# Optimization experiments

Measured on AMD Instinct MI355X. Metric: run time of the kernel, lower is better.

Reference implementation:

```python
import jax, jax.numpy as jnp
import numpy as np

K = 3
K2 = K * K


def conv2d(x, w, b, stride=1, pad=0):
    y = jax.lax.conv_general_dilated(
        x, w, (stride, stride), [(pad, pad), (pad, pad)],
        dimension_numbers=('NCHW', 'OIHW', 'NCHW'))
    return y + b[None, :, None, None]


def bilinear_gather(x, ys, xs):
    # x: [B,C,H,W]; ys,xs: [B,K2,H,W] float coords; zero outside bounds (torchvision deform_conv2d semantics)
    B, C, H, W = x.shape
    y0 = jnp.floor(ys)
    x0 = jnp.floor(xs)
    fy = (ys - y0)[:, None]  # [B,1,K2,H,W]
    fx = (xs - x0)[:, None]
    xf = x.reshape(B, C, H * W)

    def gather(yc, xc):
        valid = (yc >= 0) & (yc <= H - 1) & (xc >= 0) & (xc <= W - 1)
        yi = jnp.clip(yc, 0, H - 1).astype(jnp.int32)
        xi = jnp.clip(xc, 0, W - 1).astype(jnp.int32)
        idx = (yi * W + xi).reshape(B, 1, -1)
        g = jnp.take_along_axis(xf, idx, axis=2).reshape(B, C, K2, H, W)
        return g * valid[:, None].astype(x.dtype)

    g00 = gather(y0, x0)
    g01 = gather(y0, x0 + 1)
    g10 = gather(y0 + 1, x0)
    g11 = gather(y0 + 1, x0 + 1)
    return (g00 * (1 - fy) * (1 - fx) + g01 * (1 - fy) * fx
            + g10 * fy * (1 - fx) + g11 * fy * fx)


def deform_conv(x, w_off, b_off, w, b):
    # DCNv1: offsets predicted by a regular 3x3 conv, then 3x3 conv over bilinearly sampled taps
    B, C, H, W = x.shape
    pad = 1
    off = conv2d(x, w_off, b_off, pad=pad).reshape(B, K2, 2, H, W)  # (dy,dx) per tap
    ky, kx = jnp.meshgrid(jnp.arange(K), jnp.arange(K), indexing='ij')
    base_y = jnp.arange(H)[None, None, :, None] + (ky.reshape(K2) - pad)[None, :, None, None]
    base_x = jnp.arange(W)[None, None, None, :] + (kx.reshape(K2) - pad)[None, :, None, None]
    ys = base_y + off[:, :, 0]
    xs = base_x + off[:, :, 1]
    samples = bilinear_gather(x, ys, xs)  # [B,C,K2,H,W]
    out = jnp.einsum('bckhw,ock->bohw', samples, w.reshape(w.shape[0], C, K2))
    return out + b[None, :, None, None]


def band_high_mask(h, w):
    y, x = jnp.meshgrid(jnp.arange(h), jnp.arange(w), indexing='ij')
    d = jnp.sqrt(((y - h // 2) ** 2 + (x - w // 2) ** 2).astype(jnp.float32))
    return (d > h // 16).astype(jnp.float32)


def reference(x, w1, b1, ws, bs, wb, bb, woff, boff, wreg, breg, w2, b2):
    B, Cin, Hx, Wx = x.shape
    c0 = conv2d(x, w1, b1)                                  # 1x1 reduce
    c1 = conv2d(c0, ws, bs, stride=2, pad=0)                # 3x3 s2 p0 -> 111x111
    c1 = jax.lax.reduce_window(c1, -jnp.inf, jax.lax.max,
                               (1, 1, 7, 7), (1, 1, 3, 3), 'VALID')  # -> 35x35
    f = jnp.fft.fftshift(jnp.fft.fft2(c1, axes=(-2, -1)), axes=(-2, -1))
    mag = jnp.abs(f)
    phase = jnp.angle(f)
    h, w = mag.shape[-2], mag.shape[-1]
    hb = mag * band_high_mask(h, w)
    for l in range(3):  # fixed structural loop over the 3 DCN+ReLU blocks
        hb = jax.nn.relu(deform_conv(hb, woff[l], boff[l], wreg[l], breg[l]))
    rec = jax.lax.complex(hb * jnp.cos(phase), hb * jnp.sin(phase))
    rec = jnp.real(jnp.fft.ifft2(jnp.fft.ifftshift(rec, axes=(-2, -1)), axes=(-2, -1)))
    up = jax.image.resize(rec, (B, rec.shape[1], Hx, Wx), method='bilinear')  # align_corners=False
    c2 = jax.nn.sigmoid(conv2d(conv2d(c0, wb, bb) + up, w2, b2))
    return x * c2


def setup_inputs():
    key = jax.random.key(0)
    ks = jax.random.split(key, 8)
    B, Cin, H, W = 4, 256, 224, 224
    Cr = Cin // 8
    f32 = jnp.float32
    x = jax.random.normal(ks[0], (B, Cin, H, W), f32)
    w1 = jax.random.normal(ks[1], (Cr, Cin, 1, 1), f32) * 0.05
    b1 = jnp.zeros((Cr,), f32)
    ws = jax.random.normal(ks[2], (Cr, Cr, 3, 3), f32) * 0.05
    bs = jnp.zeros((Cr,), f32)
    wb = jax.random.normal(ks[3], (Cr, Cr, 1, 1), f32) * 0.05
    bb = jnp.zeros((Cr,), f32)
    woff = jax.random.normal(ks[4], (3, 2 * K2, Cr, 3, 3), f32) * 0.002  # small -> moderate offsets
    boff = jnp.zeros((3, 2 * K2), f32)
    wreg = jax.random.normal(ks[5], (3, Cr, Cr, 3, 3), f32) * 0.05
    breg = jnp.zeros((3, Cr), f32)
    w2 = jax.random.normal(ks[6], (Cin, Cr, 1, 1), f32) * 0.05
    b2 = jnp.zeros((Cin,), f32)
    return dict(x=x, w1=w1, b1=b1, ws=ws, bs=bs, wb=wb, bb=bb,
                woff=woff, boff=boff, wreg=wreg, breg=breg, w2=w2, b2=b2)
```

## Files before the change

kernel.cpp:

```cpp
#include <hip/hip_runtime.h>
#include <math.h>

#define PI_F 3.14159265358979323846f

#define BATCH 4
#define CIN 256
#define CR 32
#define H0 224
#define HW0 (224*224)
#define H1 111
#define HW1 (111*111)
#define HS 35
#define HWS (35*35)

typedef short bf16x8 __attribute__((ext_vector_type(8)));
typedef float f32x4 __attribute__((ext_vector_type(4)));
typedef unsigned int u32x4 __attribute__((ext_vector_type(4)));

__device__ inline unsigned pack2(float a, float b) {
  unsigned ua = __builtin_bit_cast(unsigned, a);
  unsigned ub = __builtin_bit_cast(unsigned, b);
  return ((ua + 0x8000u) >> 16) | (((ub + 0x8000u) >> 16) << 16);
}

__device__ inline bf16x8 pack8(const float f[8]) {
  u32x4 u;
  u[0] = pack2(f[0], f[1]);
  u[1] = pack2(f[2], f[3]);
  u[2] = pack2(f[4], f[5]);
  u[3] = pack2(f[6], f[7]);
  return __builtin_bit_cast(bf16x8, u);
}

__global__ __launch_bounds__(256) void k_prep(
    const float* __restrict__ w1, const float* __restrict__ b1,
    const float* __restrict__ wb, const float* __restrict__ bb,
    float* __restrict__ Wcat, float* __restrict__ bias_v) {
  __shared__ float wbl[32 * 32];
  int t = threadIdx.x;
  for (int i = t; i < 1024; i += 256) wbl[i] = wb[i];
  __syncthreads();
  float col[32];
#pragma unroll
  for (int m = 0; m < 32; ++m) col[m] = w1[m * CIN + t];
#pragma unroll
  for (int o = 0; o < 32; ++o) {
    float s = 0.f;
#pragma unroll
    for (int m = 0; m < 32; ++m) s = fmaf(wbl[o * 32 + m], col[m], s);
    Wcat[o * CIN + t] = s;
  }
  if (t < 32) {
    float s = bb[t];
#pragma unroll
    for (int m = 0; m < 32; ++m) s = fmaf(wbl[t * 32 + m], b1[m], s);
    bias_v[t] = s;
  }
}

__global__ __launch_bounds__(256) void k_conv1x1(
    const float* __restrict__ x, const float* __restrict__ w1,
    const float* __restrict__ b1, const float* __restrict__ Wcat,
    const float* __restrict__ bias_v,
    float* __restrict__ c0, float* __restrict__ v0) {
  int tid = threadIdx.x, lane = tid & 63, wid = tid >> 6;
  int l15 = lane & 15, lg = lane >> 4;
  int pxg = blockIdx.x * 256 + wid * 64;
  int b = pxg / HW0, p0 = pxg % HW0;
  f32x4 acc[4][4];
#pragma unroll
  for (int ct = 0; ct < 4; ++ct)
#pragma unroll
    for (int pt = 0; pt < 4; ++pt)
#pragma unroll
      for (int r = 0; r < 4; ++r) acc[ct][pt][r] = 0.f;
  const float* xb = x + (size_t)b * CIN * HW0 + p0 + l15;
  for (int ks = 0; ks < 8; ++ks) {
    bf16x8 Bf[4];
#pragma unroll
    for (int pt = 0; pt < 4; ++pt) {
      const float* xp = xb + (size_t)(ks * 32 + lg * 8) * HW0 + pt * 16;
      float f[8];
#pragma unroll
      for (int j = 0; j < 8; ++j) f[j] = xp[(size_t)j * HW0];
      Bf[pt] = pack8(f);
    }
    bf16x8 A[4];
#pragma unroll
    for (int ct = 0; ct < 4; ++ct) {
      const float* base = (ct < 2)
          ? w1 + (ct * 16 + l15) * CIN
          : Wcat + ((ct - 2) * 16 + l15) * CIN;
      const float* wr = base + ks * 32 + lg * 8;
      float f[8];
      float4 a0 = *reinterpret_cast<const float4*>(wr);
      float4 a1 = *reinterpret_cast<const float4*>(wr + 4);
      f[0]=a0.x; f[1]=a0.y; f[2]=a0.z; f[3]=a0.w;
      f[4]=a1.x; f[5]=a1.y; f[6]=a1.z; f[7]=a1.w;
      A[ct] = pack8(f);
    }
#pragma unroll
    for (int ct = 0; ct < 4; ++ct)
#pragma unroll
      for (int pt = 0; pt < 4; ++pt)
        acc[ct][pt] = __builtin_amdgcn_mfma_f32_16x16x32_bf16(
            A[ct], Bf[pt], acc[ct][pt], 0, 0, 0);
  }
#pragma unroll
  for (int ct = 0; ct < 4; ++ct) {
    int co = (ct & 1) * 16 + lg * 4;
    float bias[4];
#pragma unroll
    for (int r = 0; r < 4; ++r)
      bias[r] = (ct < 2) ? b1[co + r] : bias_v[co + r];
    float* dst = (ct < 2) ? c0 : v0;
    float* ob = dst + ((size_t)b * CR + co) * HW0 + p0 + l15;
#pragma unroll
    for (int pt = 0; pt < 4; ++pt)
#pragma unroll
      for (int r = 0; r < 4; ++r)
        ob[(size_t)r * HW0 + pt * 16] = acc[ct][pt][r] + bias[r];
  }
}

#define PPR 56
#define PAIRS_B (H1 * PPR)
#define PAIRS_T (BATCH * PAIRS_B)
#define C3_THREADS (PAIRS_T * 4)
__global__ __launch_bounds__(256) void k_conv3x3s2(
    const float* __restrict__ c0, const float* __restrict__ wsw,
    const float* __restrict__ bs, float* __restrict__ c1) {
  __shared__ float wl[288 * 32];
  int tid = threadIdx.x;
  for (int i = tid; i < 9216; i += 256) {
    int o = i & 31, r = i >> 5;
    wl[i] = wsw[o * 288 + r];
  }
  __syncthreads();
  int T = blockIdx.x * 256 + tid;
  if (T >= C3_THREADS) return;
  int og = T / PAIRS_T;
  int pair = T % PAIRS_T;
  int b = pair / PAIRS_B;
  int pr = pair % PAIRS_B;
  int y = pr / PPR, xp = pr % PPR;
  bool tail = (xp == PPR - 1);
  const float* ibase = c0 + (size_t)b * CR * HW0 + (2 * y) * H0 + 4 * xp;
  float acc0[8], acc1[8];
#pragma unroll
  for (int j = 0; j < 8; ++j) { acc0[j] = 0.f; acc1[j] = 0.f; }
  for (int ci = 0; ci < CR; ++ci) {
    float p[3][5];
#pragma unroll
    for (int ky = 0; ky < 3; ++ky) {
      const float* rp = ibase + (size_t)ci * HW0 + ky * H0;
      float4 v = *reinterpret_cast<const float4*>(rp);
      p[ky][0] = v.x; p[ky][1] = v.y; p[ky][2] = v.z; p[ky][3] = v.w;
      p[ky][4] = tail ? 0.f : rp[4];
    }
    const float* wbase = &wl[ci * 9 * 32 + og * 8];
#pragma unroll
    for (int k = 0; k < 9; ++k) {
      int ky = k / 3, kx = k % 3;
      float4 wa = *reinterpret_cast<const float4*>(wbase + k * 32);
      float4 wc = *reinterpret_cast<const float4*>(wbase + k * 32 + 4);
      float wv[8] = {wa.x, wa.y, wa.z, wa.w, wc.x, wc.y, wc.z, wc.w};
      float pa = p[ky][kx], pb = p[ky][kx + 2];
#pragma unroll
      for (int j = 0; j < 8; ++j) {
        acc0[j] = fmaf(pa, wv[j], acc0[j]);
        acc1[j] = fmaf(pb, wv[j], acc1[j]);
      }
    }
  }
  float* ob = c1 + (size_t)b * CR * HW1 + y * H1 + 2 * xp;
  int o0 = og * 8;
#pragma unroll
  for (int j = 0; j < 8; ++j) {
    float bias = bs[o0 + j];
    ob[(size_t)(o0 + j) * HW1] = acc0[j] + bias;
    if (!tail) ob[(size_t)(o0 + j) * HW1 + 1] = acc1[j] + bias;
  }
}

__global__ __launch_bounds__(512) void k_fft(
    const float* __restrict__ c1, float* __restrict__ hb,
    float* __restrict__ cph, float* __restrict__ sph) {
  __shared__ float p[HWS];
  __shared__ float Tr[HWS], Ti[HWS];
  __shared__ float twc[HS], tws[HS];
  int img = blockIdx.x;
  const float* cb = c1 + (size_t)img * HW1;
  for (int i = threadIdx.x; i < HWS; i += 512) {
    int y = i / HS, x = i % HS;
    const float* ip = cb + (3 * y) * H1 + 3 * x;
    float m = -INFINITY;
#pragma unroll
    for (int ky = 0; ky < 7; ++ky)
#pragma unroll
      for (int kx = 0; kx < 7; ++kx)
        m = fmaxf(m, ip[ky * H1 + kx]);
    p[i] = m;
  }
  if (threadIdx.x < HS) {
    float ang = -2.f * PI_F * (float)threadIdx.x / (float)HS;
    twc[threadIdx.x] = cosf(ang);
    tws[threadIdx.x] = sinf(ang);
  }
  __syncthreads();
  for (int i = threadIdx.x; i < HWS; i += 512) {
    int u = i / HS, xx = i % HS;
    float sr = 0.f, si = 0.f;
    int t = 0;
    for (int y = 0; y < HS; ++y) {
      float v = p[y * HS + xx];
      sr = fmaf(v, twc[t], sr);
      si = fmaf(v, tws[t], si);
      t += u; if (t >= HS) t -= HS;
    }
    Tr[i] = sr; Ti[i] = si;
  }
  __syncthreads();
  float* hp = hb + (size_t)img * HWS;
  float* cp = cph + (size_t)img * HWS;
  float* sp = sph + (size_t)img * HWS;
  for (int i = threadIdx.x; i < HWS; i += 512) {
    int oy = i / HS, ox = i % HS;
    int u = oy + 18; if (u >= HS) u -= HS;
    int v = ox + 18; if (v >= HS) v -= HS;
    float fr = 0.f, fi = 0.f;
    int t = 0;
    for (int xx = 0; xx < HS; ++xx) {
      float tr = Tr[u * HS + xx], ti = Ti[u * HS + xx];
      float c = twc[t], s = tws[t];
      fr += tr * c - ti * s;
      fi += tr * s + ti * c;
      t += v; if (t >= HS) t -= HS;
    }
    float mag = sqrtf(fr * fr + fi * fi);
    float ic = 1.f, is = 0.f;
    if (mag > 0.f) { ic = fr / mag; is = fi / mag; }
    int dy = oy - 17, dx = ox - 17;
    float m = (dy * dy + dx * dx > 4) ? 1.f : 0.f;
    hp[i] = mag * m;
    cp[i] = ic; sp[i] = is;
  }
}

__global__ __launch_bounds__(256) void k_dcn(
    const float* __restrict__ hin, float* __restrict__ hout,
    const float* __restrict__ woff, const float* __restrict__ boff,
    const float* __restrict__ wreg, const float* __restrict__ breg) {
  __shared__ float wo[18 * CR * 9];
  __shared__ float wr[CR * CR * 9];
  __shared__ float bo[18], br[CR];
  for (int i = threadIdx.x; i < 18 * CR * 9; i += 256) wo[i] = woff[i];
  for (int i = threadIdx.x; i < CR * CR * 9; i += 256) wr[i] = wreg[i];
  if (threadIdx.x < 18) bo[threadIdx.x] = boff[threadIdx.x];
  if (threadIdx.x < CR) br[threadIdx.x] = breg[threadIdx.x];
  __syncthreads();
  int pg = threadIdx.x >> 5;
  int sub = threadIdx.x & 31;
  int pid = blockIdx.x * 8 + pg;
  bool active = pid < BATCH * HWS;
  int b = pid / HWS, r = pid % HWS;
  int y = r / HS, x = r % HS;
  const float* ib = hin + (size_t)b * CR * HWS;
  float off[18];
#pragma unroll
  for (int j = 0; j < 18; ++j) off[j] = 0.f;
  if (active) {
    const float* ip = ib + (size_t)sub * HWS;
#pragma unroll
    for (int ky = 0; ky < 3; ++ky) {
      int yy = y + ky - 1;
      if (yy < 0 || yy > HS - 1) continue;
#pragma unroll
      for (int kx = 0; kx < 3; ++kx) {
        int xx = x + kx - 1;
        if (xx < 0 || xx > HS - 1) continue;
        float v = ip[yy * HS + xx];
#pragma unroll
        for (int j = 0; j < 18; ++j)
          off[j] = fmaf(v, wo[(j * CR + sub) * 9 + ky * 3 + kx], off[j]);
      }
    }
  }
#pragma unroll
  for (int d = 1; d < 32; d <<= 1)
#pragma unroll
    for (int j = 0; j < 18; ++j)
      off[j] += __shfl_xor(off[j], d);
#pragma unroll
  for (int j = 0; j < 18; ++j) off[j] += bo[j];
  float acc[CR];
#pragma unroll
  for (int o = 0; o < CR; ++o) acc[o] = 0.f;
  if (active) {
    const float* ip = ib + (size_t)sub * HWS;
#pragma unroll
    for (int k = 0; k < 9; ++k) {
      int ky = k / 3, kx = k % 3;
      float ysf = (float)(y + ky - 1) + off[2 * k];
      float xsf = (float)(x + kx - 1) + off[2 * k + 1];
      float y0 = floorf(ysf), x0 = floorf(xsf);
      float fy = ysf - y0, fx = xsf - x0;
      float y1 = y0 + 1.f, x1 = x0 + 1.f;
      bool vy0 = (y0 >= 0.f) && (y0 <= 34.f);
      bool vy1 = (y1 >= 0.f) && (y1 <= 34.f);
      bool vx0 = (x0 >= 0.f) && (x0 <= 34.f);
      bool vx1 = (x1 >= 0.f) && (x1 <= 34.f);
      int iy0 = (int)fminf(fmaxf(y0, 0.f), 34.f);
      int iy1 = (int)fminf(fmaxf(y1, 0.f), 34.f);
      int ix0 = (int)fminf(fmaxf(x0, 0.f), 34.f);
      int ix1 = (int)fminf(fmaxf(x1, 0.f), 34.f);
      float w00 = (vy0 && vx0) ? (1.f - fy) * (1.f - fx) : 0.f;
      float w01 = (vy0 && vx1) ? (1.f - fy) * fx : 0.f;
      float w10 = (vy1 && vx0) ? fy * (1.f - fx) : 0.f;
      float w11 = (vy1 && vx1) ? fy * fx : 0.f;
      float s = w00 * ip[iy0 * HS + ix0] + w01 * ip[iy0 * HS + ix1]
              + w10 * ip[iy1 * HS + ix0] + w11 * ip[iy1 * HS + ix1];
#pragma unroll
      for (int o = 0; o < CR; ++o)
        acc[o] = fmaf(s, wr[(o * CR + sub) * 9 + k], acc[o]);
    }
  }
#pragma unroll
  for (int d = 1; d < 32; d <<= 1)
#pragma unroll
    for (int o = 0; o < CR; ++o)
      acc[o] += __shfl_xor(acc[o], d);
  if (active) {
    float* ob = hout + (size_t)b * CR * HWS + r;
    float v = acc[sub] + br[sub];
    ob[(size_t)sub * HWS] = fmaxf(v, 0.f);
  }
}

__global__ __launch_bounds__(512) void k_ifft(
    const float* __restrict__ hb, const float* __restrict__ cph,
    const float* __restrict__ sph, float* __restrict__ rec) {
  __shared__ float Gr[HWS], Gi[HWS];
  __shared__ float Tr[HWS], Ti[HWS];
  __shared__ float twc[HS], tws[HS];
  int img = blockIdx.x;
  const float* hp = hb + (size_t)img * HWS;
  const float* cp = cph + (size_t)img * HWS;
  const float* sp = sph + (size_t)img * HWS;
  if (threadIdx.x < HS) {
    float ang = 2.f * PI_F * (float)threadIdx.x / (float)HS;
    twc[threadIdx.x] = cosf(ang);
    tws[threadIdx.x] = sinf(ang);
  }
  for (int i = threadIdx.x; i < HWS; i += 512) {
    int m = i / HS, n = i % HS;
    int sm = m + 17; if (sm >= HS) sm -= HS;
    int sn = n + 17; if (sn >= HS) sn -= HS;
    int si = sm * HS + sn;
    float h = hp[si];
    Gr[i] = h * cp[si];
    Gi[i] = h * sp[si];
  }
  __syncthreads();
  for (int i = threadIdx.x; i < HWS; i += 512) {
    int yy = i / HS, v = i % HS;
    float sr = 0.f, sii = 0.f;
    int t = 0;
    for (int u = 0; u < HS; ++u) {
      float gr = Gr[u * HS + v], gi = Gi[u * HS + v];
      float c = twc[t], s = tws[t];
      sr += gr * c - gi * s;
      sii += gr * s + gi * c;
      t += yy; if (t >= HS) t -= HS;
    }
    Tr[i] = sr; Ti[i] = sii;
  }
  __syncthreads();
  float* rp = rec + (size_t)img * HWS;
  const float inv = 1.f / (float)(HWS);
  for (int i = threadIdx.x; i < HWS; i += 512) {
    int yy = i / HS, xx = i % HS;
    float sr = 0.f;
    int t = 0;
    for (int v = 0; v < HS; ++v) {
      sr += Tr[yy * HS + v] * twc[t] - Ti[yy * HS + v] * tws[t];
      t += xx; if (t >= HS) t -= HS;
    }
    rp[i] = sr * inv;
  }
}

__global__ __launch_bounds__(256) void k_final(
    const float* __restrict__ x, const float* __restrict__ v0buf,
    const float* __restrict__ rec,
    const float* __restrict__ w2, const float* __restrict__ b2,
    float* __restrict__ out) {
  int tid = threadIdx.x, lane = tid & 63, wid = tid >> 6;
  int l15 = lane & 15, lg = lane >> 4;
  int pxg = blockIdx.x * 256 + wid * 64;
  int b = pxg / HW0, p0 = pxg % HW0;
  int ctb = blockIdx.y * 64;
  const float* rb = rec + (size_t)b * CR * HWS;
  const float* vb = v0buf + (size_t)b * CR * HW0 + p0 + l15;
  const float scale = (float)HS / (float)H0;
  bf16x8 Bf[4];
#pragma unroll
  for (int pt = 0; pt < 4; ++pt) {
    int p = p0 + pt * 16 + l15;
    int h = p / H0, wc = p % H0;
    float sy = ((float)h + 0.5f) * scale - 0.5f;
    float sx = ((float)wc + 0.5f) * scale - 0.5f;
    float y0f = floorf(sy), x0f = floorf(sx);
    float fy = sy - y0f, fx = sx - x0f;
    int y0 = max(0, min(HS - 1, (int)y0f));
    int y1 = max(0, min(HS - 1, (int)y0f + 1));
    int x0 = max(0, min(HS - 1, (int)x0f));
    int x1 = max(0, min(HS - 1, (int)x0f + 1));
    float w00 = (1.f - fy) * (1.f - fx), w01 = (1.f - fy) * fx;
    float w10 = fy * (1.f - fx), w11 = fy * fx;
    int i00 = y0 * HS + x0, i01 = y0 * HS + x1;
    int i10 = y1 * HS + x0, i11 = y1 * HS + x1;
    float f[8];
#pragma unroll
    for (int j = 0; j < 8; ++j) {
      const float* rp = rb + (size_t)(lg * 8 + j) * HWS;
      float u = w00 * rp[i00] + w01 * rp[i01] + w10 * rp[i10] + w11 * rp[i11];
      f[j] = vb[(size_t)(lg * 8 + j) * HW0 + pt * 16] + u;
    }
    Bf[pt] = pack8(f);
  }
  bf16x8 A[4];
#pragma unroll
  for (int ct = 0; ct < 4; ++ct) {
    const float* wr = w2 + (ctb + ct * 16 + l15) * CR + lg * 8;
    float f[8];
    float4 a0 = *reinterpret_cast<const float4*>(wr);
    float4 a1 = *reinterpret_cast<const float4*>(wr + 4);
    f[0]=a0.x; f[1]=a0.y; f[2]=a0.z; f[3]=a0.w;
    f[4]=a1.x; f[5]=a1.y; f[6]=a1.z; f[7]=a1.w;
    A[ct] = pack8(f);
  }
  f32x4 acc[4][4];
#pragma unroll
  for (int ct = 0; ct < 4; ++ct)
#pragma unroll
    for (int pt = 0; pt < 4; ++pt)
#pragma unroll
      for (int r = 0; r < 4; ++r) acc[ct][pt][r] = 0.f;
#pragma unroll
  for (int ct = 0; ct < 4; ++ct)
#pragma unroll
    for (int pt = 0; pt < 4; ++pt)
      acc[ct][pt] = __builtin_amdgcn_mfma_f32_16x16x32_bf16(
          A[ct], Bf[pt], acc[ct][pt], 0, 0, 0);
#pragma unroll
  for (int ct = 0; ct < 4; ++ct) {
    int co = ctb + ct * 16 + lg * 4;
    float bias[4];
#pragma unroll
    for (int r = 0; r < 4; ++r) bias[r] = b2[co + r];
    const float* xb = x + ((size_t)b * CIN + co) * HW0 + p0 + l15;
    float* ob = out + ((size_t)b * CIN + co) * HW0 + p0 + l15;
#pragma unroll
    for (int pt = 0; pt < 4; ++pt)
#pragma unroll
      for (int r = 0; r < 4; ++r) {
        float s = acc[ct][pt][r] + bias[r];
        float g = __builtin_amdgcn_rcpf(1.f + __expf(-s));
        ob[(size_t)r * HW0 + pt * 16] = xb[(size_t)r * HW0 + pt * 16] * g;
      }
  }
}

extern "C" void kernel_launch(void* const* d_in, const int* in_sizes, int n_in,
                              void* d_out, int out_size, void* d_ws, size_t ws_size,
                              hipStream_t stream) {
  const float* x    = (const float*)d_in[0];
  const float* w1   = (const float*)d_in[1];
  const float* b1   = (const float*)d_in[2];
  const float* wsw  = (const float*)d_in[3];
  const float* bs   = (const float*)d_in[4];
  const float* wb   = (const float*)d_in[5];
  const float* bb   = (const float*)d_in[6];
  const float* woff = (const float*)d_in[7];
  const float* boff = (const float*)d_in[8];
  const float* wreg = (const float*)d_in[9];
  const float* breg = (const float*)d_in[10];
  const float* w2   = (const float*)d_in[11];
  const float* b2   = (const float*)d_in[12];
  float* out = (float*)d_out;

  float* ws_f = (float*)d_ws;
  float* c0   = ws_f;
  float* v0   = c0 + (size_t)BATCH * CR * HW0;
  float* c1   = v0 + (size_t)BATCH * CR * HW0;
  float* hbA  = c1 + (size_t)BATCH * CR * HW1;
  float* hbB  = hbA + (size_t)BATCH * CR * HWS;
  float* cph  = hbB + (size_t)BATCH * CR * HWS;
  float* sph  = cph + (size_t)BATCH * CR * HWS;
  float* rec  = sph + (size_t)BATCH * CR * HWS;
  float* Wcat = rec + (size_t)BATCH * CR * HWS;
  float* bias_v = Wcat + 32 * CIN;

  k_prep<<<1, 256, 0, stream>>>(w1, b1, wb, bb, Wcat, bias_v);
  k_conv1x1<<<BATCH * HW0 / 256, 256, 0, stream>>>(x, w1, b1, Wcat, bias_v, c0, v0);
  k_conv3x3s2<<<(C3_THREADS + 255) / 256, 256, 0, stream>>>(c0, wsw, bs, c1);
  k_fft<<<BATCH * CR, 512, 0, stream>>>(c1, hbA, cph, sph);
  k_dcn<<<(BATCH * HWS + 7) / 8, 256, 0, stream>>>(hbA, hbB, woff, boff, wreg, breg);
  k_dcn<<<(BATCH * HWS + 7) / 8, 256, 0, stream>>>(hbB, hbA, woff + 5184, boff + 18, wreg + 9216, breg + 32);
  k_dcn<<<(BATCH * HWS + 7) / 8, 256, 0, stream>>>(hbA, hbB, woff + 2 * 5184, boff + 36, wreg + 2 * 9216, breg + 64);
  k_ifft<<<BATCH * CR, 512, 0, stream>>>(hbB, cph, sph, rec);
  dim3 gf(BATCH * HW0 / 256, 4);
  k_final<<<gf, 256, 0, stream>>>(x, v0, rec, w2, b2, out);
}
```

Before: 337.8 us.

## Split FFT/IFFT per image across two blocks, move upsample-add into separate kernel

The FFT and IFFT kernels now launch two blocks per image, each computing only the rows its half of the output needs, so the grid has twice as many blocks. The bilinear upsample of the reconstruction is taken out of the final kernel into a new k_up kernel that adds it into v0 in place. The final MFMA kernel then reads v0 only and covers 32 output channels per block instead of 64, over twice as many blocks. The cost is one extra launch and an extra read-modify-write pass over v0. In exchange the final kernel no longer repeats the upsample for every channel-group block.

```diff
diff --git a/kernel.cpp b/kernel.cpp
--- a/kernel.cpp
+++ b/kernel.cpp
@@ -189,7 +189,11 @@
   __shared__ float p[HWS];
   __shared__ float Tr[HWS], Ti[HWS];
   __shared__ float twc[HS], tws[HS];
-  int img = blockIdx.x;
+  int img = blockIdx.x >> 1;
+  int half = blockIdx.x & 1;
+  int ub = half ? 0 : 18;
+  int un = half ? 18 : 17;
+  int oyb = half ? 17 : 0;
   const float* cb = c1 + (size_t)img * HW1;
   for (int i = threadIdx.x; i < HWS; i += 512) {
     int y = i / HS, x = i % HS;
@@ -208,8 +212,8 @@
     tws[threadIdx.x] = sinf(ang);
   }
   __syncthreads();
-  for (int i = threadIdx.x; i < HWS; i += 512) {
-    int u = i / HS, xx = i % HS;
+  for (int i = threadIdx.x; i < un * HS; i += 512) {
+    int u = ub + i / HS, xx = i % HS;
     float sr = 0.f, si = 0.f;
     int t = 0;
     for (int y = 0; y < HS; ++y) {
@@ -218,14 +222,14 @@
       si = fmaf(v, tws[t], si);
       t += u; if (t >= HS) t -= HS;
     }
-    Tr[i] = sr; Ti[i] = si;
+    Tr[u * HS + xx] = sr; Ti[u * HS + xx] = si;
   }
   __syncthreads();
   float* hp = hb + (size_t)img * HWS;
   float* cp = cph + (size_t)img * HWS;
   float* sp = sph + (size_t)img * HWS;
-  for (int i = threadIdx.x; i < HWS; i += 512) {
-    int oy = i / HS, ox = i % HS;
+  for (int i = threadIdx.x; i < un * HS; i += 512) {
+    int oy = oyb + i / HS, ox = i % HS;
     int u = oy + 18; if (u >= HS) u -= HS;
     int v = ox + 18; if (v >= HS) v -= HS;
     float fr = 0.f, fi = 0.f;
@@ -242,8 +246,9 @@
     if (mag > 0.f) { ic = fr / mag; is = fi / mag; }
     int dy = oy - 17, dx = ox - 17;
     float m = (dy * dy + dx * dx > 4) ? 1.f : 0.f;
-    hp[i] = mag * m;
-    cp[i] = ic; sp[i] = is;
+    int o = oy * HS + ox;
+    hp[o] = mag * m;
+    cp[o] = ic; sp[o] = is;
   }
 }
 
@@ -343,7 +348,10 @@
   __shared__ float Gr[HWS], Gi[HWS];
   __shared__ float Tr[HWS], Ti[HWS];
   __shared__ float twc[HS], tws[HS];
-  int img = blockIdx.x;
+  int img = blockIdx.x >> 1;
+  int half = blockIdx.x & 1;
+  int yb = half ? 18 : 0;
+  int yn = half ? 17 : 18;
   const float* hp = hb + (size_t)img * HWS;
   const float* cp = cph + (size_t)img * HWS;
   const float* sp = sph + (size_t)img * HWS;
@@ -362,8 +370,8 @@
     Gi[i] = h * sp[si];
   }
   __syncthreads();
-  for (int i = threadIdx.x; i < HWS; i += 512) {
-    int yy = i / HS, v = i % HS;
+  for (int i = threadIdx.x; i < yn * HS; i += 512) {
+    int yy = yb + i / HS, v = i % HS;
     float sr = 0.f, sii = 0.f;
     int t = 0;
     for (int u = 0; u < HS; ++u) {
@@ -373,65 +381,72 @@
       sii += gr * s + gi * c;
       t += yy; if (t >= HS) t -= HS;
     }
-    Tr[i] = sr; Ti[i] = sii;
+    Tr[yy * HS + v] = sr; Ti[yy * HS + v] = sii;
   }
   __syncthreads();
   float* rp = rec + (size_t)img * HWS;
   const float inv = 1.f / (float)(HWS);
-  for (int i = threadIdx.x; i < HWS; i += 512) {
-    int yy = i / HS, xx = i % HS;
+  for (int i = threadIdx.x; i < yn * HS; i += 512) {
+    int yy = yb + i / HS, xx = i % HS;
     float sr = 0.f;
     int t = 0;
     for (int v = 0; v < HS; ++v) {
       sr += Tr[yy * HS + v] * twc[t] - Ti[yy * HS + v] * tws[t];
       t += xx; if (t >= HS) t -= HS;
     }
-    rp[i] = sr * inv;
+    rp[yy * HS + xx] = sr * inv;
+  }
+}
+
+__global__ __launch_bounds__(256) void k_up(
+    float* __restrict__ v0, const float* __restrict__ rec) {
+  int pix = blockIdx.x * 256 + threadIdx.x;
+  int b = pix / HW0, p = pix % HW0;
+  int h = p / H0, wc = p % H0;
+  const float scale = (float)HS / (float)H0;
+  float sy = ((float)h + 0.5f) * scale - 0.5f;
+  float sx = ((float)wc + 0.5f) * scale - 0.5f;
+  float y0f = floorf(sy), x0f = floorf(sx);
+  float fy = sy - y0f, fx = sx - x0f;
+  int y0 = max(0, min(HS - 1, (int)y0f));
+  int y1 = max(0, min(HS - 1, (int)y0f + 1));
+  int x0 = max(0, min(HS - 1, (int)x0f));
+  int x1 = max(0, min(HS - 1, (int)x0f + 1));
+  float w00 = (1.f - fy) * (1.f - fx), w01 = (1.f - fy) * fx;
+  float w10 = fy * (1.f - fx), w11 = fy * fx;
+  const float* rb = rec + (size_t)b * CR * HWS;
+  int i00 = y0 * HS + x0, i01 = y0 * HS + x1, i10 = y1 * HS + x0, i11 = y1 * HS + x1;
+  float* vb = v0 + (size_t)b * CR * HW0 + p;
+#pragma unroll
+  for (int cr = 0; cr < CR; ++cr) {
+    const float* rp = rb + (size_t)cr * HWS;
+    float u = w00 * rp[i00] + w01 * rp[i01] + w10 * rp[i10] + w11 * rp[i11];
+    vb[(size_t)cr * HW0] += u;
   }
 }
 
 __global__ __launch_bounds__(256) void k_final(
     const float* __restrict__ x, const float* __restrict__ v0buf,
-    const float* __restrict__ rec,
     const float* __restrict__ w2, const float* __restrict__ b2,
     float* __restrict__ out) {
   int tid = threadIdx.x, lane = tid & 63, wid = tid >> 6;
   int l15 = lane & 15, lg = lane >> 4;
   int pxg = blockIdx.x * 256 + wid * 64;
   int b = pxg / HW0, p0 = pxg % HW0;
-  int ctb = blockIdx.y * 64;
-  const float* rb = rec + (size_t)b * CR * HWS;
+  int ctb = blockIdx.y * 32;
   const float* vb = v0buf + (size_t)b * CR * HW0 + p0 + l15;
-  const float scale = (float)HS / (float)H0;
   bf16x8 Bf[4];
 #pragma unroll
   for (int pt = 0; pt < 4; ++pt) {
-    int p = p0 + pt * 16 + l15;
-    int h = p / H0, wc = p % H0;
-    float sy = ((float)h + 0.5f) * scale - 0.5f;
-    float sx = ((float)wc + 0.5f) * scale - 0.5f;
-    float y0f = floorf(sy), x0f = floorf(sx);
-    float fy = sy - y0f, fx = sx - x0f;
-    int y0 = max(0, min(HS - 1, (int)y0f));
-    int y1 = max(0, min(HS - 1, (int)y0f + 1));
-    int x0 = max(0, min(HS - 1, (int)x0f));
-    int x1 = max(0, min(HS - 1, (int)x0f + 1));
-    float w00 = (1.f - fy) * (1.f - fx), w01 = (1.f - fy) * fx;
-    float w10 = fy * (1.f - fx), w11 = fy * fx;
-    int i00 = y0 * HS + x0, i01 = y0 * HS + x1;
-    int i10 = y1 * HS + x0, i11 = y1 * HS + x1;
     float f[8];
 #pragma unroll
-    for (int j = 0; j < 8; ++j) {
-      const float* rp = rb + (size_t)(lg * 8 + j) * HWS;
-      float u = w00 * rp[i00] + w01 * rp[i01] + w10 * rp[i10] + w11 * rp[i11];
-      f[j] = vb[(size_t)(lg * 8 + j) * HW0 + pt * 16] + u;
-    }
+    for (int j = 0; j < 8; ++j)
+      f[j] = vb[(size_t)(lg * 8 + j) * HW0 + pt * 16];
     Bf[pt] = pack8(f);
   }
-  bf16x8 A[4];
-#pragma unroll
-  for (int ct = 0; ct < 4; ++ct) {
+  bf16x8 A[2];
+#pragma unroll
+  for (int ct = 0; ct < 2; ++ct) {
     const float* wr = w2 + (ctb + ct * 16 + l15) * CR + lg * 8;
     float f[8];
     float4 a0 = *reinterpret_cast<const float4*>(wr);
@@ -440,21 +455,21 @@
     f[4]=a1.x; f[5]=a1.y; f[6]=a1.z; f[7]=a1.w;
     A[ct] = pack8(f);
   }
-  f32x4 acc[4][4];
-#pragma unroll
-  for (int ct = 0; ct < 4; ++ct)
+  f32x4 acc[2][4];
+#pragma unroll
+  for (int ct = 0; ct < 2; ++ct)
 #pragma unroll
     for (int pt = 0; pt < 4; ++pt)
 #pragma unroll
       for (int r = 0; r < 4; ++r) acc[ct][pt][r] = 0.f;
 #pragma unroll
-  for (int ct = 0; ct < 4; ++ct)
+  for (int ct = 0; ct < 2; ++ct)
 #pragma unroll
     for (int pt = 0; pt < 4; ++pt)
       acc[ct][pt] = __builtin_amdgcn_mfma_f32_16x16x32_bf16(
           A[ct], Bf[pt], acc[ct][pt], 0, 0, 0);
 #pragma unroll
-  for (int ct = 0; ct < 4; ++ct) {
+  for (int ct = 0; ct < 2; ++ct) {
     int co = ctb + ct * 16 + lg * 4;
     float bias[4];
 #pragma unroll
@@ -505,11 +520,12 @@
   k_prep<<<1, 256, 0, stream>>>(w1, b1, wb, bb, Wcat, bias_v);
   k_conv1x1<<<BATCH * HW0 / 256, 256, 0, stream>>>(x, w1, b1, Wcat, bias_v, c0, v0);
   k_conv3x3s2<<<(C3_THREADS + 255) / 256, 256, 0, stream>>>(c0, wsw, bs, c1);
-  k_fft<<<BATCH * CR, 512, 0, stream>>>(c1, hbA, cph, sph);
+  k_fft<<<BATCH * CR * 2, 512, 0, stream>>>(c1, hbA, cph, sph);
   k_dcn<<<(BATCH * HWS + 7) / 8, 256, 0, stream>>>(hbA, hbB, woff, boff, wreg, breg);
   k_dcn<<<(BATCH * HWS + 7) / 8, 256, 0, stream>>>(hbB, hbA, woff + 5184, boff + 18, wreg + 9216, breg + 32);
   k_dcn<<<(BATCH * HWS + 7) / 8, 256, 0, stream>>>(hbA, hbB, woff + 2 * 5184, boff + 36, wreg + 2 * 9216, breg + 64);
-  k_ifft<<<BATCH * CR, 512, 0, stream>>>(hbB, cph, sph, rec);
-  dim3 gf(BATCH * HW0 / 256, 4);
-  k_final<<<gf, 256, 0, stream>>>(x, v0, rec, w2, b2, out);
-}
+  k_ifft<<<BATCH * CR * 2, 512, 0, stream>>>(hbB, cph, sph, rec);
+  k_up<<<BATCH * HW0 / 256, 256, 0, stream>>>(v0, rec);
+  dim3 gf(BATCH * HW0 / 256, 8);
+  k_final<<<gf, 256, 0, stream>>>(x, v0, w2, b2, out);
+}
```

Result: slower. 409.8 us (+21.3%).

## Share upsampled B-tile across output-channel waves via LDS in final kernel

Applied to the files above, without the earlier changes.

The final fused 1x1 conv kernel now builds the bilinear-upsampled plus v0 input tile for 64 pixels once per block and stores it as packed bf16 in shared memory. Each of the four waves then covers a different 64-channel slice of the 256 outputs. Before, the grid's y dimension recomputed the same B operand four times, once per channel block. This removes redundant v0 and rec reads and interpolation math, at the cost of a barrier and an LDS round trip.

```diff
diff --git a/kernel.cpp b/kernel.cpp
--- a/kernel.cpp
+++ b/kernel.cpp
@@ -395,19 +395,15 @@
     const float* __restrict__ rec,
     const float* __restrict__ w2, const float* __restrict__ b2,
     float* __restrict__ out) {
-  int tid = threadIdx.x, lane = tid & 63, wid = tid >> 6;
-  int l15 = lane & 15, lg = lane >> 4;
-  int pxg = blockIdx.x * 256 + wid * 64;
+  __shared__ unsigned Bls[64 * 20];
+  int tid = threadIdx.x;
+  int pxg = blockIdx.x * 64;
   int b = pxg / HW0, p0 = pxg % HW0;
-  int ctb = blockIdx.y * 64;
-  const float* rb = rec + (size_t)b * CR * HWS;
-  const float* vb = v0buf + (size_t)b * CR * HW0 + p0 + l15;
-  const float scale = (float)HS / (float)H0;
-  bf16x8 Bf[4];
-#pragma unroll
-  for (int pt = 0; pt < 4; ++pt) {
-    int p = p0 + pt * 16 + l15;
+  {
+    int px = tid & 63, half = tid >> 6;
+    int p = p0 + px;
     int h = p / H0, wc = p % H0;
+    const float scale = (float)HS / (float)H0;
     float sy = ((float)h + 0.5f) * scale - 0.5f;
     float sx = ((float)wc + 0.5f) * scale - 0.5f;
     float y0f = floorf(sy), x0f = floorf(sx);
@@ -420,14 +416,31 @@
     float w10 = fy * (1.f - fx), w11 = fy * fx;
     int i00 = y0 * HS + x0, i01 = y0 * HS + x1;
     int i10 = y1 * HS + x0, i11 = y1 * HS + x1;
+    const float* rb = rec + ((size_t)b * CR + half * 8) * HWS;
+    const float* vb = v0buf + ((size_t)b * CR + half * 8) * HW0 + p;
     float f[8];
 #pragma unroll
     for (int j = 0; j < 8; ++j) {
-      const float* rp = rb + (size_t)(lg * 8 + j) * HWS;
+      const float* rp = rb + (size_t)j * HWS;
       float u = w00 * rp[i00] + w01 * rp[i01] + w10 * rp[i10] + w11 * rp[i11];
-      f[j] = vb[(size_t)(lg * 8 + j) * HW0 + pt * 16] + u;
-    }
-    Bf[pt] = pack8(f);
+      f[j] = vb[(size_t)j * HW0] + u;
+    }
+    u32x4 u4;
+    u4[0] = pack2(f[0], f[1]);
+    u4[1] = pack2(f[2], f[3]);
+    u4[2] = pack2(f[4], f[5]);
+    u4[3] = pack2(f[6], f[7]);
+    *reinterpret_cast<u32x4*>(&Bls[px * 20 + half * 4]) = u4;
+  }
+  __syncthreads();
+  int lane = tid & 63, wid = tid >> 6;
+  int l15 = lane & 15, lg = lane >> 4;
+  int ctb = wid * 64;
+  bf16x8 Bf[4];
+#pragma unroll
+  for (int pt = 0; pt < 4; ++pt) {
+    u32x4 u4 = *reinterpret_cast<const u32x4*>(&Bls[(pt * 16 + l15) * 20 + lg * 4]);
+    Bf[pt] = __builtin_bit_cast(bf16x8, u4);
   }
   bf16x8 A[4];
 #pragma unroll
@@ -510,6 +523,6 @@
   k_dcn<<<(BATCH * HWS + 7) / 8, 256, 0, stream>>>(hbB, hbA, woff + 5184, boff + 18, wreg + 9216, breg + 32);
   k_dcn<<<(BATCH * HWS + 7) / 8, 256, 0, stream>>>(hbA, hbB, woff + 2 * 5184, boff + 36, wreg + 2 * 9216, breg + 64);
   k_ifft<<<BATCH * CR, 512, 0, stream>>>(hbB, cph, sph, rec);
-  dim3 gf(BATCH * HW0 / 256, 4);
+  dim3 gf(BATCH * HW0 / 64, 1);
   k_final<<<gf, 256, 0, stream>>>(x, v0, rec, w2, b2, out);
 }
```

After: 333.4 us. No clear change (-1.3%).
